# Kernel tuning notes

Hardware: AMD Instinct MI355X
Metric: run time of the kernel (lower is better)

The kernel has to match this reference:

```python
import jax, jax.numpy as jnp
import numpy as np

NUM_NODES = 50000
NUM_EDGES = 800000
NUM_GRAPHS = 1024
D_IN = 64
D_PROT = 1280
HID = 256
OUT = 1


def setup_inputs() -> dict:
    key = jax.random.key(0)
    ks = jax.random.split(key, 16)
    s = 0.02
    x = jax.random.normal(ks[0], (NUM_NODES, D_IN), dtype=jnp.float32)
    edge_index = jax.random.randint(ks[1], (2, NUM_EDGES), 0, NUM_NODES, dtype=jnp.int32)
    batch = jnp.sort(jax.random.randint(ks[2], (NUM_NODES,), 0, NUM_GRAPHS, dtype=jnp.int32))
    protein_embedding = jax.random.normal(ks[3], (NUM_GRAPHS, D_PROT), dtype=jnp.float32)
    # SAGEConv params: lin_l (aggregated neighbors, with bias), lin_r (self, no bias)
    Wl = jax.random.normal(ks[4], (D_IN, HID), dtype=jnp.float32) * s
    bl = jnp.zeros((HID,), dtype=jnp.float32)
    Wr = jax.random.normal(ks[5], (D_IN, HID), dtype=jnp.float32) * s
    Wp = jax.random.normal(ks[6], (D_PROT, HID), dtype=jnp.float32) * s
    bp = jnp.zeros((HID,), dtype=jnp.float32)
    Wi = jax.random.normal(ks[7], (2 * HID, HID), dtype=jnp.float32) * s
    bi = jnp.zeros((HID,), dtype=jnp.float32)
    Wo = jax.random.normal(ks[8], (HID, OUT), dtype=jnp.float32) * s
    bo = jnp.zeros((OUT,), dtype=jnp.float32)
    return {"x": x, "protein_embedding": protein_embedding, "Wl": Wl, "bl": bl,
            "Wr": Wr, "Wp": Wp, "bp": bp, "Wi": Wi, "bi": bi, "Wo": Wo, "bo": bo,
            "edge_index": edge_index, "batch": batch}


def _segment_mean(vals, seg_ids, num_segments):
    sums = jax.ops.segment_sum(vals, seg_ids, num_segments=num_segments)
    cnt = jax.ops.segment_sum(jnp.ones((vals.shape[0],), vals.dtype), seg_ids,
                              num_segments=num_segments)
    return sums / jnp.maximum(cnt, 1.0)[:, None]


def reference(x, protein_embedding, Wl, bl, Wr, Wp, bp, Wi, bi, Wo, bo, edge_index, batch):
    src, dst = edge_index[0], edge_index[1]
    # SAGEConv: mean-aggregate neighbor messages at target nodes, then fuse linears
    aggr = _segment_mean(x[src], dst, NUM_NODES)           # [N, D_IN]
    drug_x = jax.nn.relu(aggr @ Wl + bl + x @ Wr)          # [N, HID]
    # global_mean_pool over graphs in the batch
    pooled = _segment_mean(drug_x, batch, NUM_GRAPHS)      # [G, HID]
    protein_x = protein_embedding @ Wp + bp                # [G, HID]
    combined = jnp.concatenate((pooled, protein_x), axis=1)  # [G, 2*HID]
    interaction = jax.nn.relu(combined @ Wi + bi)          # [G, HID]
    return interaction @ Wo + bo                           # [G, OUT]
```

## Files before the change

kernel.cpp:

```cpp
#include <hip/hip_runtime.h>
#include <hip/hip_bf16.h>

#define N_NODES 50000
#define N_EDGES 800000
#define N_GRAPHS 1024
#define D_IN 64
#define D_PROT 1280
#define HID 256
#define N_PAD 50048

#define NB 782
#define BCAP 2048
#define BEPB 4096
#define BBLK 196

typedef __attribute__((ext_vector_type(8))) short short8;
typedef __attribute__((ext_vector_type(4))) float f32x4;
typedef __hip_bfloat16 bf16;

__device__ inline unsigned bf16rne(float f) {
  unsigned u = __float_as_uint(f);
  return (u + 0x7fffu + ((u >> 16) & 1u)) >> 16;
}
__device__ inline void acc_bf2(float4& a, uint2 v) {
  a.x += __uint_as_float(v.x << 16);
  a.y += __uint_as_float(v.x & 0xffff0000u);
  a.z += __uint_as_float(v.y << 16);
  a.w += __uint_as_float(v.y & 0xffff0000u);
}

#define PREP_XC 3125
#define PREP_PE (PREP_XC + 1280)
#define PREP_PL (PREP_PE + 8)
#define PREP_PR (PREP_PL + 8)
#define PREP_WP (PREP_PR + 160)
#define PREP_WI (PREP_WP + 64)
#define PREP_GB (PREP_WI + 196)

__device__ inline void pack_frag(const float* __restrict__ src, bf16* __restrict__ dst,
                                 int KC, int tid) {
  int lane = tid & 63;
  int chunk = tid >> 6;
  int c = chunk / KC, kc = chunk - c * KC;
  int kbase = kc * 32 + ((lane >> 4) * 8);
  int n = c * 16 + (lane & 15);
#pragma unroll
  for (int j = 0; j < 8; ++j)
    dst[(size_t)tid * 8 + j] = __float2bfloat16(src[(size_t)(kbase + j) * HID + n]);
}

__global__ __launch_bounds__(256) void k_front(
    const float* __restrict__ x, const float* __restrict__ pe,
    const float* __restrict__ Wl, const float* __restrict__ Wr,
    const float* __restrict__ Wp, const float* __restrict__ Wi,
    const int* __restrict__ ei, const int* __restrict__ batch,
    uint2* __restrict__ x2, uint2* __restrict__ pe2,
    bf16* __restrict__ Wl_pk, bf16* __restrict__ Wr_pk,
    bf16* __restrict__ Wp_pk, bf16* __restrict__ Wi_pk,
    int* __restrict__ bcnt, unsigned* __restrict__ bped,
    int* __restrict__ gb) {
  __shared__ int hist[NB];
  __shared__ int base[NB];
  const int b = blockIdx.x;
  const int t = threadIdx.x;
  if (b < BBLK) {
    const int e0 = b * BEPB;
    for (int i = t; i < NB; i += 256) hist[i] = 0;
    __syncthreads();
    int dc[16];
#pragma unroll
    for (int o = 0; o < 4; ++o)
#pragma unroll
      for (int u = 0; u < 4; ++u) {
        int e = e0 + o * 1024 + u * 256 + t;
        dc[o * 4 + u] = (e < N_EDGES) ? ei[N_EDGES + e] : -1;
      }
#pragma unroll
    for (int j = 0; j < 16; ++j)
      if (dc[j] >= 0) atomicAdd(&hist[dc[j] >> 6], 1);
    __syncthreads();
    for (int i = t; i < NB; i += 256) {
      int c = hist[i];
      base[i] = (c > 0) ? atomicAdd(&bcnt[i], c) : 0;
      hist[i] = 0;
    }
    __syncthreads();
#pragma unroll
    for (int o = 0; o < 4; ++o) {
      int sc[4];
#pragma unroll
      for (int u = 0; u < 4; ++u) {
        int e = e0 + o * 1024 + u * 256 + t;
        sc[u] = (e < N_EDGES) ? ei[e] : 0;
      }
#pragma unroll
      for (int u = 0; u < 4; ++u) {
        int d = dc[o * 4 + u];
        if (d >= 0) {
          int bk = d >> 6;
          int pos = base[bk] + atomicAdd(&hist[bk], 1);
          if (pos < BCAP)
            bped[(size_t)bk * BCAP + pos] =
                (unsigned)sc[u] | ((unsigned)(d & 63) << 16);
        }
      }
    }
    return;
  }
  const int pb = b - BBLK;
  if (pb < PREP_XC) {
    int tid = pb * 256 + t;
    float4 v = ((const float4*)x)[tid];
    x2[tid] = make_uint2(bf16rne(v.x) | (bf16rne(v.y) << 16),
                         bf16rne(v.z) | (bf16rne(v.w) << 16));
  } else if (pb < PREP_PE) {
    int tid = (pb - PREP_XC) * 256 + t;
    float4 v = ((const float4*)pe)[tid];
    pe2[tid] = make_uint2(bf16rne(v.x) | (bf16rne(v.y) << 16),
                          bf16rne(v.z) | (bf16rne(v.w) << 16));
  } else if (pb < PREP_PL) {
    pack_frag(Wl, Wl_pk, 2, (pb - PREP_PE) * 256 + t);
  } else if (pb < PREP_PR) {
    pack_frag(Wr, Wr_pk, 2, (pb - PREP_PL) * 256 + t);
  } else if (pb < PREP_WP) {
    pack_frag(Wp, Wp_pk, 40, (pb - PREP_PR) * 256 + t);
  } else if (pb < PREP_WI) {
    pack_frag(Wi, Wi_pk, 16, (pb - PREP_WP) * 256 + t);
  } else {
    int n = (pb - PREP_WI) * 256 + t;
    if (n < N_NODES) {
      int bc = batch[n];
      int bprev = (n == 0) ? -1 : batch[n - 1];
      for (int g = bprev + 1; g <= bc; ++g) gb[g] = n;
      if (n == N_NODES - 1)
        for (int g = bc + 1; g <= N_GRAPHS; ++g) gb[g] = N_NODES;
    }
  }
}

__global__ __launch_bounds__(256) void k_mid(
    const uint2* __restrict__ x2, const unsigned* __restrict__ bped,
    const int* __restrict__ bcnt, uint2* __restrict__ a2,
    const bf16* __restrict__ pebf, const bf16* __restrict__ Wp_pk,
    const float* __restrict__ bp, unsigned short* __restrict__ comb) {
  __shared__ unsigned short s_e[BCAP];
  __shared__ int s_off[65];
  __shared__ int s_cur[64];
  const int t = threadIdx.x;
  const int w = t >> 6, lane = t & 63;
  const int ml = lane & 15, q = lane >> 4;
  if (blockIdx.x < NB) {
    const int b = blockIdx.x;
    const int nE = min(bcnt[b], BCAP);
    const unsigned* bpp = bped + (size_t)b * BCAP;
    if (t < 64) s_cur[t] = 0;
    __syncthreads();
    for (int i = t; i < nE; i += 256)
      atomicAdd(&s_cur[(bpp[i] >> 16) & 63], 1);
    __syncthreads();
    if (t < 64) {
      int sc = s_cur[t];
#pragma unroll
      for (int off = 1; off < 64; off <<= 1) {
        int u = __shfl_up(sc, off);
        if (t >= off) sc += u;
      }
      s_off[t + 1] = sc;
      if (t == 0) s_off[0] = 0;
      s_cur[t] = 0;
    }
    __syncthreads();
    for (int i = t; i < nE; i += 256) {
      unsigned pk = bpp[i];
      int ld = (pk >> 16) & 63;
      int pos = s_off[ld] + atomicAdd(&s_cur[ld], 1);
      s_e[pos] = (unsigned short)(pk & 0xffffu);
    }
    __syncthreads();

    const int el = q & 3;
    const int fb = ml;
    for (int n = w; n < 64; n += 4) {
      const int beg = s_off[n], end = s_off[n + 1];
      float4 s0 = {0,0,0,0}, s1 = {0,0,0,0}, s2 = {0,0,0,0}, s3 = {0,0,0,0};
      int e = beg;
      for (; e + 16 <= end; e += 16) {
        int i0 = s_e[e + el],     i1 = s_e[e + 4 + el];
        int i2 = s_e[e + 8 + el], i3 = s_e[e + 12 + el];
        uint2 v0 = x2[(size_t)i0 * 16 + fb];
        uint2 v1 = x2[(size_t)i1 * 16 + fb];
        uint2 v2 = x2[(size_t)i2 * 16 + fb];
        uint2 v3 = x2[(size_t)i3 * 16 + fb];
        acc_bf2(s0, v0); acc_bf2(s1, v1); acc_bf2(s2, v2); acc_bf2(s3, v3);
      }
      for (; e + 4 <= end; e += 4)
        acc_bf2(s0, x2[(size_t)s_e[e + el] * 16 + fb]);
      if (e + el < end)
        acc_bf2(s1, x2[(size_t)s_e[e + el] * 16 + fb]);
      float4 tt;
      tt.x = (s0.x + s1.x) + (s2.x + s3.x);
      tt.y = (s0.y + s1.y) + (s2.y + s3.y);
      tt.z = (s0.z + s1.z) + (s2.z + s3.z);
      tt.w = (s0.w + s1.w) + (s2.w + s3.w);
      tt.x += __shfl_xor(tt.x, 32); tt.x += __shfl_xor(tt.x, 16);
      tt.y += __shfl_xor(tt.y, 32); tt.y += __shfl_xor(tt.y, 16);
      tt.z += __shfl_xor(tt.z, 32); tt.z += __shfl_xor(tt.z, 16);
      tt.w += __shfl_xor(tt.w, 32); tt.w += __shfl_xor(tt.w, 16);
      const int node = b * 64 + n;
      if (el == 0 && node < N_NODES) {
        float inv = 1.0f / (float)max(end - beg, 1);
        uint2 o;
        o.x = bf16rne(tt.x * inv) | (bf16rne(tt.y * inv) << 16);
        o.y = bf16rne(tt.z * inv) | (bf16rne(tt.w * inv) << 16);
        a2[(size_t)node * 16 + fb] = o;
      }
    }
    return;
  }
  const int g0 = (blockIdx.x - NB) * 16;
  f32x4 acc[4];
#pragma unroll
  for (int c = 0; c < 4; ++c) acc[c] = (f32x4){0.f, 0.f, 0.f, 0.f};
  for (int kc = 0; kc < 40; ++kc) {
    short8 a = *(const short8*)(pebf + (size_t)(g0 + ml) * D_PROT + kc * 32 + q * 8);
#pragma unroll
    for (int cl = 0; cl < 4; ++cl) {
      short8 bb = *(const short8*)(Wp_pk + ((size_t)((w * 4 + cl) * 40 + kc) * 64 + lane) * 8);
      acc[cl] = __builtin_amdgcn_mfma_f32_16x16x32_bf16(a, bb, acc[cl], 0, 0, 0);
    }
  }
#pragma unroll
  for (int cl = 0; cl < 4; ++cl) {
    const int col = w * 64 + cl * 16 + ml;
    const float bias = bp[col];
#pragma unroll
    for (int i = 0; i < 4; ++i)
      comb[(size_t)(g0 + q * 4 + i) * 512 + HID + col] =
          (unsigned short)bf16rne(acc[cl][i] + bias);
  }
}

__global__ __launch_bounds__(256) void k_mlp(
    const bf16* __restrict__ aggrbf, const bf16* __restrict__ xbf,
    const bf16* __restrict__ Wl_pk, const bf16* __restrict__ Wr_pk,
    const float* __restrict__ bl, unsigned short* __restrict__ drug) {
  const int t = threadIdx.x, w = t >> 6, lane = t & 63;
  const int ml = lane & 15, q = lane >> 4;
  const int n0 = blockIdx.x * 64;

  f32x4 acc[4][4];
#pragma unroll
  for (int a = 0; a < 4; ++a)
#pragma unroll
    for (int c = 0; c < 4; ++c) acc[a][c] = (f32x4){0.f, 0.f, 0.f, 0.f};

#pragma unroll
  for (int mat = 0; mat < 2; ++mat) {
    const bf16* A = mat ? xbf : aggrbf;
    const bf16* B = mat ? Wr_pk : Wl_pk;
#pragma unroll
    for (int kc = 0; kc < 2; ++kc) {
      short8 af[4], bfr[4];
#pragma unroll
      for (int rt = 0; rt < 4; ++rt)
        af[rt] = *(const short8*)(A + (size_t)(n0 + rt * 16 + ml) * D_IN + kc * 32 + q * 8);
#pragma unroll
      for (int cl = 0; cl < 4; ++cl)
        bfr[cl] = *(const short8*)(B + ((size_t)((w * 4 + cl) * 2 + kc) * 64 + lane) * 8);
#pragma unroll
      for (int rt = 0; rt < 4; ++rt)
#pragma unroll
        for (int cl = 0; cl < 4; ++cl)
          acc[rt][cl] = __builtin_amdgcn_mfma_f32_16x16x32_bf16(af[rt], bfr[cl], acc[rt][cl], 0, 0, 0);
    }
  }

#pragma unroll
  for (int cl = 0; cl < 4; ++cl) {
    const int col = w * 64 + cl * 16 + ml;
    const float bias = bl[col];
#pragma unroll
    for (int rt = 0; rt < 4; ++rt) {
#pragma unroll
      for (int i = 0; i < 4; ++i) {
        const int row = n0 + rt * 16 + q * 4 + i;
        drug[(size_t)row * HID + col] =
            (unsigned short)bf16rne(fmaxf(acc[rt][cl][i] + bias, 0.f));
      }
    }
  }
}

__global__ __launch_bounds__(256) void k_pool(
    const unsigned short* __restrict__ drug, const int* __restrict__ gb,
    unsigned short* __restrict__ comb) {
  const int g = blockIdx.x, t = threadIdx.x;
  const int lo = gb[g], hi = gb[g + 1];
  float s0 = 0.f, s1 = 0.f, s2 = 0.f, s3 = 0.f;
  float s4 = 0.f, s5 = 0.f, s6 = 0.f, s7 = 0.f;
  int r = lo;
  for (; r + 8 <= hi; r += 8) {
    s0 += __uint_as_float((unsigned)drug[(size_t)(r + 0) * HID + t] << 16);
    s1 += __uint_as_float((unsigned)drug[(size_t)(r + 1) * HID + t] << 16);
    s2 += __uint_as_float((unsigned)drug[(size_t)(r + 2) * HID + t] << 16);
    s3 += __uint_as_float((unsigned)drug[(size_t)(r + 3) * HID + t] << 16);
    s4 += __uint_as_float((unsigned)drug[(size_t)(r + 4) * HID + t] << 16);
    s5 += __uint_as_float((unsigned)drug[(size_t)(r + 5) * HID + t] << 16);
    s6 += __uint_as_float((unsigned)drug[(size_t)(r + 6) * HID + t] << 16);
    s7 += __uint_as_float((unsigned)drug[(size_t)(r + 7) * HID + t] << 16);
  }
  for (; r < hi; ++r)
    s0 += __uint_as_float((unsigned)drug[(size_t)r * HID + t] << 16);
  float inv = 1.0f / (float)max(hi - lo, 1);
  float m = (((s0 + s1) + (s2 + s3)) + ((s4 + s5) + (s6 + s7))) * inv;
  comb[(size_t)g * 512 + t] = (unsigned short)bf16rne(m);
}

__global__ __launch_bounds__(256) void k_tail(
    const bf16* __restrict__ comb, const bf16* __restrict__ Wi_pk,
    const float* __restrict__ bi, const float* __restrict__ Wo,
    const float* __restrict__ bo, float* __restrict__ out) {
  __shared__ float sRed[16 * 4];
  const int t = threadIdx.x, w = t >> 6, lane = t & 63;
  const int ml = lane & 15, q = lane >> 4;
  const int g0 = blockIdx.x * 16;
  f32x4 acc[4];
#pragma unroll
  for (int c = 0; c < 4; ++c) acc[c] = (f32x4){0.f, 0.f, 0.f, 0.f};
  for (int kc = 0; kc < 16; ++kc) {
    short8 a = *(const short8*)(comb + (size_t)(g0 + ml) * 512 + kc * 32 + q * 8);
#pragma unroll
    for (int cl = 0; cl < 4; ++cl) {
      short8 bb = *(const short8*)(Wi_pk + ((size_t)((w * 4 + cl) * 16 + kc) * 64 + lane) * 8);
      acc[cl] = __builtin_amdgcn_mfma_f32_16x16x32_bf16(a, bb, acc[cl], 0, 0, 0);
    }
  }
  float bic[4], woc[4];
#pragma unroll
  for (int cl = 0; cl < 4; ++cl) {
    const int col = w * 64 + cl * 16 + ml;
    bic[cl] = bi[col];
    woc[cl] = Wo[col];
  }
#pragma unroll
  for (int i = 0; i < 4; ++i) {
    float s = 0.f;
#pragma unroll
    for (int cl = 0; cl < 4; ++cl)
      s += fmaxf(acc[cl][i] + bic[cl], 0.f) * woc[cl];
    s += __shfl_xor(s, 1); s += __shfl_xor(s, 2);
    s += __shfl_xor(s, 4); s += __shfl_xor(s, 8);
    if (ml == 0) sRed[(q * 4 + i) * 4 + w] = s;
  }
  __syncthreads();
  if (t < 16)
    out[g0 + t] = sRed[t * 4 + 0] + sRed[t * 4 + 1] + sRed[t * 4 + 2]
                + sRed[t * 4 + 3] + bo[0];
}

extern "C" void kernel_launch(void* const* d_in, const int* in_sizes, int n_in,
                              void* d_out, int out_size, void* d_ws, size_t ws_size,
                              hipStream_t stream) {
  const float* x     = (const float*)d_in[0];
  const float* pe    = (const float*)d_in[1];
  const float* Wl    = (const float*)d_in[2];
  const float* bl    = (const float*)d_in[3];
  const float* Wr    = (const float*)d_in[4];
  const float* Wp    = (const float*)d_in[5];
  const float* bp    = (const float*)d_in[6];
  const float* Wi    = (const float*)d_in[7];
  const float* bi    = (const float*)d_in[8];
  const float* Wo    = (const float*)d_in[9];
  const float* bo    = (const float*)d_in[10];
  const int*   ei    = (const int*)d_in[11];
  const int*   batch = (const int*)d_in[12];
  float* out = (float*)d_out;

  char* p = (char*)d_ws;
  auto alloc = [&](size_t bytes) {
    char* r = p;
    p += (bytes + 255) & ~(size_t)255;
    return r;
  };
  int*      bcnt  = (int*)alloc(NB * 4);
  size_t zbytes = (size_t)(p - (char*)d_ws);
  unsigned* bped  = (unsigned*)alloc((size_t)NB * BCAP * 4);
  bf16*  xbf    = (bf16*)alloc((size_t)N_PAD * D_IN * 2);
  bf16*  aggrbf = (bf16*)alloc((size_t)N_PAD * D_IN * 2);
  bf16*  pebf   = (bf16*)alloc((size_t)N_GRAPHS * D_PROT * 2);
  bf16*  Wl_pk  = (bf16*)alloc((size_t)D_IN * HID * 2);
  bf16*  Wr_pk  = (bf16*)alloc((size_t)D_IN * HID * 2);
  bf16*  Wp_pk  = (bf16*)alloc((size_t)D_PROT * HID * 2);
  bf16*  Wi_pk  = (bf16*)alloc((size_t)2 * HID * HID * 2);
  int*   gb     = (int*)alloc((N_GRAPHS + 1) * 4);
  unsigned short* drug = (unsigned short*)alloc((size_t)N_PAD * HID * 2);
  unsigned short* comb = (unsigned short*)alloc((size_t)N_GRAPHS * 2 * HID * 2);

  (void)hipMemsetAsync(d_ws, 0, zbytes, stream);

  k_front<<<BBLK + PREP_GB, 256, 0, stream>>>(
      x, pe, Wl, Wr, Wp, Wi, ei, batch,
      (uint2*)xbf, (uint2*)pebf, Wl_pk, Wr_pk, Wp_pk, Wi_pk, bcnt, bped, gb);
  k_mid<<<NB + 64, 256, 0, stream>>>(
      (const uint2*)xbf, bped, bcnt, (uint2*)aggrbf, pebf, Wp_pk, bp,
      comb);
  k_mlp<<<N_PAD / 64, 256, 0, stream>>>(aggrbf, xbf, Wl_pk, Wr_pk, bl, drug);
  k_pool<<<N_GRAPHS, 256, 0, stream>>>(drug, gb, comb);
  k_tail<<<N_GRAPHS / 16, 256, 0, stream>>>((const bf16*)comb, Wi_pk, bi, Wo, bo, out);
}
```

Baseline: 182.0 us.

## Split bucket sort and neighbor gather into separate kernels; move protein GEMM into MLP

```diff
diff --git a/kernel.cpp b/kernel.cpp
--- a/kernel.cpp
+++ b/kernel.cpp
@@ -138,122 +138,134 @@
   }
 }
 
-__global__ __launch_bounds__(256) void k_mid(
-    const uint2* __restrict__ x2, const unsigned* __restrict__ bped,
-    const int* __restrict__ bcnt, uint2* __restrict__ a2,
-    const bf16* __restrict__ pebf, const bf16* __restrict__ Wp_pk,
-    const float* __restrict__ bp, unsigned short* __restrict__ comb) {
+__global__ __launch_bounds__(256) void k_sort(
+    const unsigned* __restrict__ bped, const int* __restrict__ bcnt,
+    unsigned short* __restrict__ esorted, int* __restrict__ eoff) {
+  __shared__ unsigned s_raw[BCAP];
   __shared__ unsigned short s_e[BCAP];
   __shared__ int s_off[65];
   __shared__ int s_cur[64];
-  const int t = threadIdx.x;
-  const int w = t >> 6, lane = t & 63;
-  const int ml = lane & 15, q = lane >> 4;
-  if (blockIdx.x < NB) {
-    const int b = blockIdx.x;
-    const int nE = min(bcnt[b], BCAP);
-    const unsigned* bpp = bped + (size_t)b * BCAP;
-    if (t < 64) s_cur[t] = 0;
-    __syncthreads();
-    for (int i = t; i < nE; i += 256)
-      atomicAdd(&s_cur[(bpp[i] >> 16) & 63], 1);
-    __syncthreads();
-    if (t < 64) {
-      int sc = s_cur[t];
-#pragma unroll
-      for (int off = 1; off < 64; off <<= 1) {
-        int u = __shfl_up(sc, off);
-        if (t >= off) sc += u;
-      }
-      s_off[t + 1] = sc;
-      if (t == 0) s_off[0] = 0;
-      s_cur[t] = 0;
-    }
-    __syncthreads();
-    for (int i = t; i < nE; i += 256) {
-      unsigned pk = bpp[i];
-      int ld = (pk >> 16) & 63;
-      int pos = s_off[ld] + atomicAdd(&s_cur[ld], 1);
-      s_e[pos] = (unsigned short)(pk & 0xffffu);
-    }
-    __syncthreads();
-
-    const int el = q & 3;
-    const int fb = ml;
-    for (int n = w; n < 64; n += 4) {
-      const int beg = s_off[n], end = s_off[n + 1];
-      float4 s0 = {0,0,0,0}, s1 = {0,0,0,0}, s2 = {0,0,0,0}, s3 = {0,0,0,0};
-      int e = beg;
-      for (; e + 16 <= end; e += 16) {
-        int i0 = s_e[e + el],     i1 = s_e[e + 4 + el];
-        int i2 = s_e[e + 8 + el], i3 = s_e[e + 12 + el];
-        uint2 v0 = x2[(size_t)i0 * 16 + fb];
-        uint2 v1 = x2[(size_t)i1 * 16 + fb];
-        uint2 v2 = x2[(size_t)i2 * 16 + fb];
-        uint2 v3 = x2[(size_t)i3 * 16 + fb];
-        acc_bf2(s0, v0); acc_bf2(s1, v1); acc_bf2(s2, v2); acc_bf2(s3, v3);
-      }
-      for (; e + 4 <= end; e += 4)
-        acc_bf2(s0, x2[(size_t)s_e[e + el] * 16 + fb]);
-      if (e + el < end)
-        acc_bf2(s1, x2[(size_t)s_e[e + el] * 16 + fb]);
-      float4 tt;
-      tt.x = (s0.x + s1.x) + (s2.x + s3.x);
-      tt.y = (s0.y + s1.y) + (s2.y + s3.y);
-      tt.z = (s0.z + s1.z) + (s2.z + s3.z);
-      tt.w = (s0.w + s1.w) + (s2.w + s3.w);
-      tt.x += __shfl_xor(tt.x, 32); tt.x += __shfl_xor(tt.x, 16);
-      tt.y += __shfl_xor(tt.y, 32); tt.y += __shfl_xor(tt.y, 16);
-      tt.z += __shfl_xor(tt.z, 32); tt.z += __shfl_xor(tt.z, 16);
-      tt.w += __shfl_xor(tt.w, 32); tt.w += __shfl_xor(tt.w, 16);
-      const int node = b * 64 + n;
-      if (el == 0 && node < N_NODES) {
-        float inv = 1.0f / (float)max(end - beg, 1);
-        uint2 o;
-        o.x = bf16rne(tt.x * inv) | (bf16rne(tt.y * inv) << 16);
-        o.y = bf16rne(tt.z * inv) | (bf16rne(tt.w * inv) << 16);
-        a2[(size_t)node * 16 + fb] = o;
-      }
-    }
-    return;
-  }
-  const int g0 = (blockIdx.x - NB) * 16;
-  f32x4 acc[4];
-#pragma unroll
-  for (int c = 0; c < 4; ++c) acc[c] = (f32x4){0.f, 0.f, 0.f, 0.f};
-  for (int kc = 0; kc < 40; ++kc) {
-    short8 a = *(const short8*)(pebf + (size_t)(g0 + ml) * D_PROT + kc * 32 + q * 8);
-#pragma unroll
-    for (int cl = 0; cl < 4; ++cl) {
-      short8 bb = *(const short8*)(Wp_pk + ((size_t)((w * 4 + cl) * 40 + kc) * 64 + lane) * 8);
-      acc[cl] = __builtin_amdgcn_mfma_f32_16x16x32_bf16(a, bb, acc[cl], 0, 0, 0);
-    }
-  }
-#pragma unroll
-  for (int cl = 0; cl < 4; ++cl) {
-    const int col = w * 64 + cl * 16 + ml;
-    const float bias = bp[col];
-#pragma unroll
-    for (int i = 0; i < 4; ++i)
-      comb[(size_t)(g0 + q * 4 + i) * 512 + HID + col] =
-          (unsigned short)bf16rne(acc[cl][i] + bias);
+  const int t = threadIdx.x, b = blockIdx.x;
+  const int nE = min(bcnt[b], BCAP);
+  if (t < 64) s_cur[t] = 0;
+  __syncthreads();
+  for (int i = t; i < nE; i += 256) {
+    unsigned pk = bped[(size_t)b * BCAP + i];
+    s_raw[i] = pk;
+    atomicAdd(&s_cur[(pk >> 16) & 63], 1);
+  }
+  __syncthreads();
+  if (t < 64) {
+    int sc = s_cur[t];
+#pragma unroll
+    for (int off = 1; off < 64; off <<= 1) {
+      int u = __shfl_up(sc, off);
+      if (t >= off) sc += u;
+    }
+    s_off[t + 1] = sc;
+    if (t == 0) s_off[0] = 0;
+    s_cur[t] = 0;
+  }
+  __syncthreads();
+  for (int i = t; i < nE; i += 256) {
+    unsigned pk = s_raw[i];
+    int ld = (pk >> 16) & 63;
+    int pos = s_off[ld] + atomicAdd(&s_cur[ld], 1);
+    s_e[pos] = (unsigned short)(pk & 0xffffu);
+  }
+  __syncthreads();
+  for (int i = t; i < nE; i += 256)
+    esorted[(size_t)b * BCAP + i] = s_e[i];
+  if (t < 65) eoff[b * 65 + t] = s_off[t];
+}
+
+__global__ __launch_bounds__(256) void k_gather(
+    const uint2* __restrict__ x2, const unsigned short* __restrict__ esorted,
+    const int* __restrict__ eoff, uint2* __restrict__ a2) {
+  const int t = threadIdx.x, w = t >> 6, lane = t & 63;
+  const int el = lane >> 4, fb = lane & 15;
+  const int b = blockIdx.x >> 2;
+  const int nbase = (blockIdx.x & 3) * 16 + w * 4;
+  const unsigned short* ep = esorted + (size_t)b * BCAP;
+  const int* eo = eoff + b * 65;
+#pragma unroll
+  for (int k = 0; k < 4; ++k) {
+    const int n = nbase + k;
+    const int beg = eo[n], end = eo[n + 1];
+    float4 s0 = {0,0,0,0}, s1 = {0,0,0,0}, s2 = {0,0,0,0}, s3 = {0,0,0,0};
+    int e = beg;
+    for (; e + 16 <= end; e += 16) {
+      int i0 = ep[e + el],     i1 = ep[e + 4 + el];
+      int i2 = ep[e + 8 + el], i3 = ep[e + 12 + el];
+      uint2 v0 = x2[(size_t)i0 * 16 + fb];
+      uint2 v1 = x2[(size_t)i1 * 16 + fb];
+      uint2 v2 = x2[(size_t)i2 * 16 + fb];
+      uint2 v3 = x2[(size_t)i3 * 16 + fb];
+      acc_bf2(s0, v0); acc_bf2(s1, v1); acc_bf2(s2, v2); acc_bf2(s3, v3);
+    }
+    for (; e + 4 <= end; e += 4)
+      acc_bf2(s0, x2[(size_t)ep[e + el] * 16 + fb]);
+    if (e + el < end)
+      acc_bf2(s1, x2[(size_t)ep[e + el] * 16 + fb]);
+    float4 tt;
+    tt.x = (s0.x + s1.x) + (s2.x + s3.x);
+    tt.y = (s0.y + s1.y) + (s2.y + s3.y);
+    tt.z = (s0.z + s1.z) + (s2.z + s3.z);
+    tt.w = (s0.w + s1.w) + (s2.w + s3.w);
+    tt.x += __shfl_xor(tt.x, 32); tt.x += __shfl_xor(tt.x, 16);
+    tt.y += __shfl_xor(tt.y, 32); tt.y += __shfl_xor(tt.y, 16);
+    tt.z += __shfl_xor(tt.z, 32); tt.z += __shfl_xor(tt.z, 16);
+    tt.w += __shfl_xor(tt.w, 32); tt.w += __shfl_xor(tt.w, 16);
+    const int node = b * 64 + n;
+    if (el == 0 && node < N_NODES) {
+      float inv = 1.0f / (float)max(end - beg, 1);
+      uint2 o;
+      o.x = bf16rne(tt.x * inv) | (bf16rne(tt.y * inv) << 16);
+      o.y = bf16rne(tt.z * inv) | (bf16rne(tt.w * inv) << 16);
+      a2[(size_t)node * 16 + fb] = o;
+    }
   }
 }
 
 __global__ __launch_bounds__(256) void k_mlp(
     const bf16* __restrict__ aggrbf, const bf16* __restrict__ xbf,
     const bf16* __restrict__ Wl_pk, const bf16* __restrict__ Wr_pk,
-    const float* __restrict__ bl, unsigned short* __restrict__ drug) {
+    const float* __restrict__ bl,
+    const bf16* __restrict__ pebf, const bf16* __restrict__ Wp_pk,
+    const float* __restrict__ bp,
+    unsigned short* __restrict__ drug, unsigned short* __restrict__ comb) {
   const int t = threadIdx.x, w = t >> 6, lane = t & 63;
   const int ml = lane & 15, q = lane >> 4;
-  const int n0 = blockIdx.x * 64;
-
+  if (blockIdx.x < 64) {
+    const int g0 = blockIdx.x * 16;
+    f32x4 acc[4];
+#pragma unroll
+    for (int c = 0; c < 4; ++c) acc[c] = (f32x4){0.f, 0.f, 0.f, 0.f};
+    for (int kc = 0; kc < 40; ++kc) {
+      short8 a = *(const short8*)(pebf + (size_t)(g0 + ml) * D_PROT + kc * 32 + q * 8);
+#pragma unroll
+      for (int cl = 0; cl < 4; ++cl) {
+        short8 bb = *(const short8*)(Wp_pk + ((size_t)((w * 4 + cl) * 40 + kc) * 64 + lane) * 8);
+        acc[cl] = __builtin_amdgcn_mfma_f32_16x16x32_bf16(a, bb, acc[cl], 0, 0, 0);
+      }
+    }
+#pragma unroll
+    for (int cl = 0; cl < 4; ++cl) {
+      const int col = w * 64 + cl * 16 + ml;
+      const float bias = bp[col];
+#pragma unroll
+      for (int i = 0; i < 4; ++i)
+        comb[(size_t)(g0 + q * 4 + i) * 512 + HID + col] =
+            (unsigned short)bf16rne(acc[cl][i] + bias);
+    }
+    return;
+  }
+  const int n0 = (blockIdx.x - 64) * 64;
   f32x4 acc[4][4];
 #pragma unroll
   for (int a = 0; a < 4; ++a)
 #pragma unroll
     for (int c = 0; c < 4; ++c) acc[a][c] = (f32x4){0.f, 0.f, 0.f, 0.f};
-
 #pragma unroll
   for (int mat = 0; mat < 2; ++mat) {
     const bf16* A = mat ? xbf : aggrbf;
@@ -274,7 +286,6 @@
           acc[rt][cl] = __builtin_amdgcn_mfma_f32_16x16x32_bf16(af[rt], bfr[cl], acc[rt][cl], 0, 0, 0);
     }
   }
-
 #pragma unroll
   for (int cl = 0; cl < 4; ++cl) {
     const int col = w * 64 + cl * 16 + ml;
@@ -385,6 +396,8 @@
   int*      bcnt  = (int*)alloc(NB * 4);
   size_t zbytes = (size_t)(p - (char*)d_ws);
   unsigned* bped  = (unsigned*)alloc((size_t)NB * BCAP * 4);
+  unsigned short* esorted = (unsigned short*)alloc((size_t)NB * BCAP * 2);
+  int*   eoff   = (int*)alloc((size_t)NB * 65 * 4);
   bf16*  xbf    = (bf16*)alloc((size_t)N_PAD * D_IN * 2);
   bf16*  aggrbf = (bf16*)alloc((size_t)N_PAD * D_IN * 2);
   bf16*  pebf   = (bf16*)alloc((size_t)N_GRAPHS * D_PROT * 2);
@@ -401,10 +414,11 @@
   k_front<<<BBLK + PREP_GB, 256, 0, stream>>>(
       x, pe, Wl, Wr, Wp, Wi, ei, batch,
       (uint2*)xbf, (uint2*)pebf, Wl_pk, Wr_pk, Wp_pk, Wi_pk, bcnt, bped, gb);
-  k_mid<<<NB + 64, 256, 0, stream>>>(
-      (const uint2*)xbf, bped, bcnt, (uint2*)aggrbf, pebf, Wp_pk, bp,
-      comb);
-  k_mlp<<<N_PAD / 64, 256, 0, stream>>>(aggrbf, xbf, Wl_pk, Wr_pk, bl, drug);
+  k_sort<<<NB, 256, 0, stream>>>(bped, bcnt, esorted, eoff);
+  k_gather<<<NB * 4, 256, 0, stream>>>(
+      (const uint2*)xbf, esorted, eoff, (uint2*)aggrbf);
+  k_mlp<<<64 + NB, 256, 0, stream>>>(
+      aggrbf, xbf, Wl_pk, Wr_pk, bl, pebf, Wp_pk, bp, drug, comb);
   k_pool<<<N_GRAPHS, 256, 0, stream>>>(drug, gb, comb);
   k_tail<<<N_GRAPHS / 16, 256, 0, stream>>>((const bf16*)comb, Wi_pk, bi, Wo, bo, out);
 }
```

Measured after the change: 178.1 us. 1.02x faster.
